# Kernel tuning notes

Measured on AMD Instinct MI355X. Metric: run time of the kernel, lower is better.

Reference implementation:

```python
import jax, jax.numpy as jnp
import numpy as np

B, S, H, M, E = 64, 512, 1024, 26, 676  # batch, seq, hidden, max_nodes, max_edges (M*M)


def setup_inputs() -> dict:
    key = jax.random.key(0)
    ks = jax.random.split(key, 16)
    seq = jax.random.normal(ks[0], (B, S, H), jnp.float32)
    # ragged, strictly-increasing sentence-end offsets in [1, S-1], zero-padded tail
    rng = np.random.RandomState(0)
    off = np.zeros((B, M - 1), np.int64)
    for b in range(B):
        c = rng.randint(5, M)  # count of valid offsets per sample (ragged)
        off[b, :c] = np.sort(rng.choice(np.arange(1, S), size=c, replace=False))
    s = 1.0 / np.sqrt(H)
    s3 = 1.0 / np.sqrt(3 * H)
    return {
        'sequence_outputs': seq,
        'proof_offsets': jnp.asarray(off),
        'node_labels': jax.random.randint(ks[1], (B, M), 0, 2),
        'edge_labels': jax.random.randint(ks[2], (B, E), 0, 2),
        'W_naf': jax.random.normal(ks[3], (H, H), jnp.float32) * s,
        'b_naf': jnp.zeros((H,), jnp.float32),
        'W_cd': jax.random.normal(ks[4], (H, H), jnp.float32) * s,
        'b_cd': jnp.zeros((H,), jnp.float32),
        'W_co': jax.random.normal(ks[5], (H, 2), jnp.float32) * s,
        'b_co': jnp.zeros((2,), jnp.float32),
        'W_nd': jax.random.normal(ks[6], (H, H), jnp.float32) * s,
        'b_nd': jnp.zeros((H,), jnp.float32),
        'W_no': jax.random.normal(ks[7], (H, 2), jnp.float32) * s,
        'b_no': jnp.zeros((2,), jnp.float32),
        'W_ed': jax.random.normal(ks[8], (3 * H, H), jnp.float32) * s3,
        'b_ed': jnp.zeros((H,), jnp.float32),
        'W_eo': jax.random.normal(ks[9], (H, 2), jnp.float32) * s,
        'b_eo': jnp.zeros((2,), jnp.float32),
    }


def reference(sequence_outputs, proof_offsets, node_labels, edge_labels,
              W_naf, b_naf, W_cd, b_cd, W_co, b_co,
              W_nd, b_nd, W_no, b_no, W_ed, b_ed, W_eo, b_eo):
    Bx, Sx, Hx = sequence_outputs.shape
    Mx = node_labels.shape[1]
    Ex = edge_labels.shape[1]

    cls = sequence_outputs[:, 0, :]                       # [B,H]
    naf = cls @ W_naf + b_naf                             # NAF node embedding
    logits = jnp.tanh(cls @ W_cd + b_cd) @ W_co + b_co    # RobertaClassificationHead (eval: dropout=id)

    # segment-mean pooling via inclusive prefix sums: segment j = tokens (prev_j, off_j]
    P = jnp.cumsum(sequence_outputs, axis=1)              # [B,S,H]
    off = proof_offsets                                   # [B,M-1]
    prev = jnp.concatenate([jnp.zeros((Bx, 1), off.dtype), off[:, :-1]], axis=1)
    valid = off > 0                                       # [B,M-1]
    seg_sum = (jnp.take_along_axis(P, off[..., None], axis=1)
               - jnp.take_along_axis(P, prev[..., None], axis=1))  # [B,M-1,H]
    seg_len = jnp.maximum(off - prev, 1).astype(sequence_outputs.dtype)
    seg_mean = seg_sum / seg_len[..., None] * valid[..., None]

    count = valid.sum(axis=1)                             # nodes per sample (excl. NAF)
    # node embeddings: seg means at 0..count-1, NAF at index count, zeros after
    node_full = jnp.concatenate([seg_mean, jnp.zeros((Bx, 1, Hx), seg_mean.dtype)], axis=1)  # [B,M,H]
    idx = jnp.arange(Mx)
    node_full = node_full + (idx[None, :, None] == count[:, None, None]) * naf[:, None, :]

    # all-pairs edge features over n=count+1 nodes, row-major flat k=i*n+j, zero-padded to E
    n = count + 1                                         # [B]
    k = jnp.arange(Ex)                                    # [E]
    i = jnp.clip(k[None, :] // n[:, None], 0, Mx - 1)     # [B,E]
    j = jnp.clip(k[None, :] % n[:, None], 0, Mx - 1)
    valid_e = (k[None, :] < (n * n)[:, None])[..., None]
    ni = jnp.take_along_axis(node_full, i[..., None], axis=1)  # [B,E,H]
    nj = jnp.take_along_axis(node_full, j[..., None], axis=1)
    edge = jnp.concatenate([nj, ni, nj - ni], axis=-1) * valid_e  # [B,E,3H]

    node_logits = jnp.tanh(node_full @ W_nd + b_nd) @ W_no + b_no
    edge_logits = jnp.tanh(edge @ W_ed + b_ed) @ W_eo + b_eo
    return (logits, node_logits, edge_logits)
```

## Files before the change

kernel.cpp:

```cpp
#include <hip/hip_runtime.h>
#include <hip/hip_bf16.h>

#define B_ 64
#define S_ 512
#define H_ 1024
#define M_ 26
#define E_ 676

typedef short bf16x8 __attribute__((ext_vector_type(8)));
typedef float f32x4 __attribute__((ext_vector_type(4)));

__device__ __forceinline__ void gload16(const void* g, void* l) {
    __builtin_amdgcn_global_load_lds((const __attribute__((address_space(1))) unsigned int*)g,
                                     (__attribute__((address_space(3))) unsigned int*)l,
                                     16, 0, 0);
}

__device__ __forceinline__ float tanh_fast(float x) {
    float e = __expf(2.0f * x);
    return 1.0f - 2.0f * __builtin_amdgcn_rcpf(e + 1.0f);
}

__global__ __launch_bounds__(256) void k_stage1(
    const float* __restrict__ seq, const int* __restrict__ off,
    const float* __restrict__ Wnaf, const float* __restrict__ Wcd,
    const float* __restrict__ Wnd, const float* __restrict__ Wed,
    const float* __restrict__ bed, const float* __restrict__ Weo,
    const float* __restrict__ beo,
    __hip_bfloat16* __restrict__ Wt, int* __restrict__ count,
    float* __restrict__ econ, float* __restrict__ naf, float* __restrict__ cdh,
    __hip_bfloat16* __restrict__ nodeB) {
    __shared__ __attribute__((aligned(16))) char smraw[20992];
    int bid = blockIdx.x;
    int tid = threadIdx.x;

    if (bid < 256) {
        __hip_bfloat16 (*ldsB)[40] = (__hip_bfloat16(*)[40])smraw;
        int* offs_s = (int*)(smraw + 20480);
        float* invL = (float*)(smraw + 20608);
        int b = bid >> 2, h0 = (bid & 3) * 256;
        int w = tid >> 6, l = tid & 63;

        if (tid < M_ - 1) offs_s[tid] = off[b * (M_ - 1) + tid];
        __syncthreads();
        int c = 0;
        while (c < M_ - 1 && offs_s[c] > 0) c++;
        int offmax = offs_s[c - 1];
        if (tid < 32)
            invL[tid] = (tid < c) ? 1.0f / (float)(offs_s[tid] - (tid ? offs_s[tid - 1] : 0))
                                  : 0.0f;
        int row0 = (l & 15), row1 = 16 + (l & 15);
        int offm0 = (row0 < c) ? offs_s[row0] : 0;
        int prv0  = (offm0 > 0) ? (row0 ? offs_s[row0 - 1] : 0) : 1;
        int offm1 = (row1 < c) ? offs_s[row1] : 0;
        int prv1  = (offm1 > 0) ? offs_s[row1 - 1] : 1;

        int nkt = (offmax >> 5) + 1;
        const float* sb = seq + (size_t)b * S_ * H_ + h0;
        float4 rg[8];
#pragma unroll
        for (int i = 0; i < 2; ++i)
#pragma unroll
            for (int r = 0; r < 4; ++r)
                rg[i * 4 + r] = *(const float4*)(sb + (size_t)((i * 4 + w) * 4 + r) * H_ + 4 * l);
        f32x4 acc[2][4] = {};
        int tA = (l >> 4) * 8;

        for (int kt = 0; kt < nkt; ++kt) {
            asm volatile("s_waitcnt vmcnt(0)" ::: "memory");
            ushort4 pk[2][4];
#pragma unroll
            for (int i = 0; i < 2; ++i)
#pragma unroll
                for (int q = 0; q < 4; ++q) {
                    float f0 = (q==0)?rg[i*4+0].x:(q==1)?rg[i*4+0].y:(q==2)?rg[i*4+0].z:rg[i*4+0].w;
                    float f1 = (q==0)?rg[i*4+1].x:(q==1)?rg[i*4+1].y:(q==2)?rg[i*4+1].z:rg[i*4+1].w;
                    float f2 = (q==0)?rg[i*4+2].x:(q==1)?rg[i*4+2].y:(q==2)?rg[i*4+2].z:rg[i*4+2].w;
                    float f3 = (q==0)?rg[i*4+3].x:(q==1)?rg[i*4+3].y:(q==2)?rg[i*4+3].z:rg[i*4+3].w;
                    __hip_bfloat16 __attribute__((aligned(8))) hh[4] = {
                        __float2bfloat16(f0), __float2bfloat16(f1),
                        __float2bfloat16(f2), __float2bfloat16(f3)};
                    pk[i][q] = *(const ushort4*)hh;
                }
            if (kt + 1 < nkt) {
#pragma unroll
                for (int i = 0; i < 2; ++i)
#pragma unroll
                    for (int r = 0; r < 4; ++r) {
                        int tl = (kt + 1) * 32 + (i * 4 + w) * 4 + r;
                        rg[i * 4 + r] = *(const float4*)(sb + (size_t)tl * H_ + 4 * l);
                    }
                __builtin_amdgcn_sched_barrier(0);
            }
#pragma unroll
            for (int i = 0; i < 2; ++i)
#pragma unroll
                for (int q = 0; q < 4; ++q)
                    *(ushort4*)&ldsB[4 * l + q][(i * 4 + w) * 4] = pk[i][q];
            asm volatile("s_waitcnt lgkmcnt(0)" ::: "memory");
            __builtin_amdgcn_s_barrier();
            int T0 = kt * 32;
            bf16x8 af0, af1;
#pragma unroll
            for (int i = 0; i < 8; ++i) {
                int t = T0 + tA + i;
                af0[i] = (t > prv0 && t <= offm0) ? (short)0x3F80 : (short)0;
                af1[i] = (t > prv1 && t <= offm1) ? (short)0x3F80 : (short)0;
            }
#pragma unroll
            for (int nn = 0; nn < 4; ++nn) {
                bf16x8 bfr = *(const bf16x8*)&ldsB[(w * 4 + nn) * 16 + (l & 15)][tA];
                acc[0][nn] = __builtin_amdgcn_mfma_f32_16x16x32_bf16(af0, bfr, acc[0][nn], 0, 0, 0);
                acc[1][nn] = __builtin_amdgcn_mfma_f32_16x16x32_bf16(af1, bfr, acc[1][nn], 0, 0, 0);
            }
            __builtin_amdgcn_s_barrier();
        }
#pragma unroll
        for (int mt = 0; mt < 2; ++mt)
#pragma unroll
            for (int nn = 0; nn < 4; ++nn) {
                f32x4 v = acc[mt][nn];
                int hcol = h0 + (w * 4 + nn) * 16 + (l & 15);
#pragma unroll
                for (int r = 0; r < 4; ++r) {
                    int m = mt * 16 + (l >> 4) * 4 + r;
                    if (m < M_)
                        nodeB[((size_t)(b * M_ + m)) * H_ + hcol] =
                            __float2bfloat16(v[r] * invL[m]);
                }
            }
    } else if (bid < 512) {
        float* smem = (float*)smraw;
        float (*As)[64] = (float(*)[64])smem;
        float (*Bs)[64] = (float(*)[64])(smem + 1024);
        int e = bid - 256;
        int bx = e & 31;
        int kbase = (e >> 5) * 128;
        const float* W;
        float* dst;
        int cbase;
        if (bx < 16) { W = Wnaf; dst = naf; cbase = bx * 64; }
        else         { W = Wcd;  dst = cdh; cbase = (bx - 16) * 64; }
        int tx = tid % 16, ty = tid / 16;
        float c[4][4] = {};
        int la_row = tid / 4;
        int la_k4  = (tid % 4) * 4;
        int lb_k   = tid / 16;
        int lb_c4  = (tid % 16) * 4;
        for (int k0 = 0; k0 < 128; k0 += 16) {
            float4 a = *(const float4*)(seq + (size_t)la_row * S_ * H_ + kbase + k0 + la_k4);
            *(float4*)(&Bs[lb_k][lb_c4]) =
                *(const float4*)(W + (size_t)(kbase + k0 + lb_k) * H_ + cbase + lb_c4);
            As[la_k4 + 0][la_row] = a.x;
            As[la_k4 + 1][la_row] = a.y;
            As[la_k4 + 2][la_row] = a.z;
            As[la_k4 + 3][la_row] = a.w;
            __syncthreads();
#pragma unroll
            for (int kk = 0; kk < 16; ++kk) {
                float4 av = *(const float4*)(&As[kk][ty * 4]);
                float4 bv = *(const float4*)(&Bs[kk][tx * 4]);
                c[0][0] += av.x * bv.x; c[0][1] += av.x * bv.y; c[0][2] += av.x * bv.z; c[0][3] += av.x * bv.w;
                c[1][0] += av.y * bv.x; c[1][1] += av.y * bv.y; c[1][2] += av.y * bv.z; c[1][3] += av.y * bv.w;
                c[2][0] += av.z * bv.x; c[2][1] += av.z * bv.y; c[2][2] += av.z * bv.z; c[2][3] += av.z * bv.w;
                c[3][0] += av.w * bv.x; c[3][1] += av.w * bv.y; c[3][2] += av.w * bv.z; c[3][3] += av.w * bv.w;
            }
            __syncthreads();
        }
#pragma unroll
        for (int i = 0; i < 4; ++i)
#pragma unroll
            for (int j = 0; j < 4; ++j)
                atomicAdd(dst + (size_t)(ty * 4 + i) * H_ + cbase + tx * 4 + j, c[i][j]);
    } else if (bid < 3584) {
        float (*T)[33] = (float(*)[33])smraw;
        int idx = bid - 512;
        int s = idx >> 10, rem = idx & 1023;
        int bx = rem & 31, by = rem >> 5;
        int c = tid & 31, r0 = tid >> 5;
        const int HH = H_ * H_;
#pragma unroll
        for (int i = 0; i < 4; ++i) {
            int r = r0 + 8 * i;
            size_t k = by * 32 + r, n = bx * 32 + c;
            float v;
            if (s == 0)      v = Wnd[k * H_ + n];
            else if (s == 1) v = Wed[k * H_ + n] + Wed[2 * HH + k * H_ + n];
            else             v = Wed[HH + k * H_ + n] - Wed[2 * HH + k * H_ + n];
            T[r][c] = v;
        }
        __syncthreads();
#pragma unroll
        for (int i = 0; i < 4; ++i) {
            int rr = r0 + 8 * i;
            Wt[(size_t)(s * H_ + bx * 32 + rr) * H_ + by * 32 + c] = __float2bfloat16(T[c][rr]);
        }
    } else if (bid == 3584) {
        if (tid < 64) {
            int b = tid;
            int c = 0;
            for (int m = 0; m < M_ - 1; ++m) c += (off[b * (M_ - 1) + m] > 0) ? 1 : 0;
            count[b] = c;
        }
    } else {
        float* s0 = (float*)smraw; float* s1 = (float*)smraw + 256;
        float a0 = 0.f, a1 = 0.f;
        for (int h = tid; h < H_; h += 256) {
            float t = tanh_fast(bed[h]);
            a0 += t * Weo[h * 2 + 0];
            a1 += t * Weo[h * 2 + 1];
        }
        s0[tid] = a0; s1[tid] = a1; __syncthreads();
        for (int o = 128; o > 0; o >>= 1) {
            if (tid < o) { s0[tid] += s0[tid + o]; s1[tid] += s1[tid + o]; }
            __syncthreads();
        }
        if (tid == 0) { econ[0] = s0[0] + beo[0]; econ[1] = s1[0] + beo[1]; }
    }
}

__global__ __launch_bounds__(256) void k_stage2s(
    const float* __restrict__ naf, const float* __restrict__ bnaf,
    const int* __restrict__ count, __hip_bfloat16* __restrict__ nodeB,
    const float* __restrict__ cdh, const float* __restrict__ bcd,
    const float* __restrict__ Wco, const float* __restrict__ bco,
    float* __restrict__ out) {
    __shared__ float smem[512];
    int bid = blockIdx.x;
    int tid = threadIdx.x;
    if (bid < 64) {
        int b = bid, cnt = count[b];
        float4 a = ((const float4*)(naf + (size_t)b * H_))[tid];
        float4 bb = ((const float4*)bnaf)[tid];
        __hip_bfloat16 __attribute__((aligned(8))) h[4] = {
            __float2bfloat16(a.x + bb.x), __float2bfloat16(a.y + bb.y),
            __float2bfloat16(a.z + bb.z), __float2bfloat16(a.w + bb.w)};
        *(ushort4*)(nodeB + ((size_t)(b * M_ + cnt)) * H_ + tid * 4) = *(const ushort4*)h;
    } else {
        int b = bid - 64;
        float* s0 = smem; float* s1 = smem + 256;
        float a0 = 0.f, a1 = 0.f;
        for (int h = tid; h < H_; h += 256) {
            float t = tanh_fast(cdh[(size_t)b * H_ + h] + bcd[h]);
            a0 += t * Wco[h * 2 + 0];
            a1 += t * Wco[h * 2 + 1];
        }
        s0[tid] = a0; s1[tid] = a1; __syncthreads();
        for (int o = 128; o > 0; o >>= 1) {
            if (tid < o) { s0[tid] += s0[tid + o]; s1[tid] += s1[tid + o]; }
            __syncthreads();
        }
        if (tid == 0) { out[b * 2 + 0] = s0[0] + bco[0]; out[b * 2 + 1] = s1[0] + bco[1]; }
    }
}

#define GM 1664
#define GN 3072
#define GK 1024
__global__ __launch_bounds__(256) void k_mfma(const __hip_bfloat16* __restrict__ A,
                                              const __hip_bfloat16* __restrict__ Bt,
                                              float* __restrict__ C) {
    __shared__ __hip_bfloat16 As[128 * 32];
    __shared__ __hip_bfloat16 Bs[128 * 32];
    int tid = threadIdx.x;
    int wid = tid >> 6, ln = tid & 63;
    int row0 = blockIdx.y * 128, col0 = blockIdx.x * 128;
    const __hip_bfloat16* ga = A + (size_t)(row0 + wid * 16 + (ln >> 2)) * GK + (ln & 3) * 8;
    const __hip_bfloat16* gb = Bt + (size_t)(col0 + wid * 16 + (ln >> 2)) * GK + (ln & 3) * 8;
    __hip_bfloat16* lA = As + wid * 512;
    __hip_bfloat16* lB = Bs + wid * 512;
    int mrow = (wid >> 1) * 64, ncol = (wid & 1) * 64;
    int l15 = ln & 15, l4 = ln >> 4;
    f32x4 acc[4][4] = {};
    const __hip_bfloat16* pa = As + (size_t)(mrow + l15) * 32 + l4 * 8;
    const __hip_bfloat16* pb = Bs + (size_t)(ncol + l15) * 32 + l4 * 8;
    for (int k0 = 0; k0 < GK; k0 += 32) {
        gload16(ga, lA);
        gload16(ga + 64 * GK, lA + 2048);
        gload16(gb, lB);
        gload16(gb + 64 * GK, lB + 2048);
        ga += 32; gb += 32;
        __syncthreads();
        bf16x8 af[4], bf[4];
#pragma unroll
        for (int mi = 0; mi < 4; ++mi) af[mi] = *(const bf16x8*)(pa + mi * 16 * 32);
#pragma unroll
        for (int ni = 0; ni < 4; ++ni) bf[ni] = *(const bf16x8*)(pb + ni * 16 * 32);
#pragma unroll
        for (int mi = 0; mi < 4; ++mi)
#pragma unroll
            for (int ni = 0; ni < 4; ++ni)
                acc[mi][ni] = __builtin_amdgcn_mfma_f32_16x16x32_bf16(af[mi], bf[ni],
                                                                      acc[mi][ni], 0, 0, 0);
        __syncthreads();
    }
#pragma unroll
    for (int mi = 0; mi < 4; ++mi)
#pragma unroll
        for (int ni = 0; ni < 4; ++ni) {
            f32x4 v = acc[mi][ni];
            size_t r = row0 + mrow + mi * 16 + l4 * 4;
            size_t cc = col0 + ncol + ni * 16 + l15;
            C[(r + 0) * GN + cc] = v[0];
            C[(r + 1) * GN + cc] = v[1];
            C[(r + 2) * GN + cc] = v[2];
            C[(r + 3) * GN + cc] = v[3];
        }
}

__global__ __launch_bounds__(256) void k_stage4(
    const float* __restrict__ Cm, const int* __restrict__ count,
    const float* __restrict__ bnd, const float* __restrict__ Wno,
    const float* __restrict__ bno, const float* __restrict__ bed,
    const float* __restrict__ Weo, const float* __restrict__ beo,
    const float* __restrict__ econ, float* __restrict__ out_n,
    float* __restrict__ out_e) {
    int bid = blockIdx.x;
    int wid = threadIdx.x >> 6, lane = threadIdx.x & 63;
    if (bid < 416) {
        int r = bid * 4 + wid;
        const float4* src = (const float4*)(Cm + (size_t)r * GN);
        float a0 = 0.f, a1 = 0.f;
#pragma unroll
        for (int it = 0; it < 4; ++it) {
            int h = lane * 4 + it * 256;
            float4 s = src[lane + it * 64];
            float4 bb = *(const float4*)(bnd + h);
            float t0 = tanh_fast(s.x + bb.x), t1 = tanh_fast(s.y + bb.y);
            float t2 = tanh_fast(s.z + bb.z), t3 = tanh_fast(s.w + bb.w);
            a0 += t0 * Wno[h * 2 + 0] + t1 * Wno[h * 2 + 2] + t2 * Wno[h * 2 + 4] + t3 * Wno[h * 2 + 6];
            a1 += t0 * Wno[h * 2 + 1] + t1 * Wno[h * 2 + 3] + t2 * Wno[h * 2 + 5] + t3 * Wno[h * 2 + 7];
        }
        for (int o = 32; o > 0; o >>= 1) { a0 += __shfl_down(a0, o); a1 += __shfl_down(a1, o); }
        if (lane == 0) { out_n[(size_t)r * 2 + 0] = a0 + bno[0]; out_n[(size_t)r * 2 + 1] = a1 + bno[1]; }
    } else {
        int e = bid - 416;
        int b = e >> 4;
        int wg = (e & 15) * 4 + wid;
        int n = count[b] + 1;
        int n2 = n * n;
        float4 bed4[4], w04[4], w14[4];
#pragma unroll
        for (int it = 0; it < 4; ++it) {
            int h = lane * 4 + it * 256;
            bed4[it] = *(const float4*)(bed + h);
            w04[it] = make_float4(Weo[h * 2 + 0], Weo[h * 2 + 2], Weo[h * 2 + 4], Weo[h * 2 + 6]);
            w14[it] = make_float4(Weo[h * 2 + 1], Weo[h * 2 + 3], Weo[h * 2 + 5], Weo[h * 2 + 7]);
        }
        float e0 = econ[0], e1 = econ[1];
        float b0 = beo[0], b1 = beo[1];
        for (int k = wg; k < E_; k += 64) {
            float* dst = out_e + ((size_t)b * E_ + k) * 2;
            if (k >= n2) {
                if (lane == 0) { dst[0] = e0; dst[1] = e1; }
                continue;
            }
            int i = k / n, j = k - i * n;
            const float4* U4 = (const float4*)(Cm + (size_t)(b * M_ + j) * GN + H_);
            const float4* V4 = (const float4*)(Cm + (size_t)(b * M_ + i) * GN + 2 * H_);
            float a0 = 0.f, a1 = 0.f;
#pragma unroll
            for (int it = 0; it < 4; ++it) {
                float4 u = U4[lane + it * 64];
                float4 v = V4[lane + it * 64];
                float t0 = tanh_fast(u.x + v.x + bed4[it].x);
                float t1 = tanh_fast(u.y + v.y + bed4[it].y);
                float t2 = tanh_fast(u.z + v.z + bed4[it].z);
                float t3 = tanh_fast(u.w + v.w + bed4[it].w);
                a0 += t0 * w04[it].x + t1 * w04[it].y + t2 * w04[it].z + t3 * w04[it].w;
                a1 += t0 * w14[it].x + t1 * w14[it].y + t2 * w14[it].z + t3 * w14[it].w;
            }
            for (int o = 32; o > 0; o >>= 1) { a0 += __shfl_down(a0, o); a1 += __shfl_down(a1, o); }
            if (lane == 0) { dst[0] = a0 + b0; dst[1] = a1 + b1; }
        }
    }
}

extern "C" void kernel_launch(void* const* d_in, const int* in_sizes, int n_in,
                              void* d_out, int out_size, void* d_ws, size_t ws_size,
                              hipStream_t stream) {
    const float* seq  = (const float*)d_in[0];
    const int*   off  = (const int*)d_in[1];
    const float* Wnaf = (const float*)d_in[4];  const float* bnaf = (const float*)d_in[5];
    const float* Wcd  = (const float*)d_in[6];  const float* bcd  = (const float*)d_in[7];
    const float* Wco  = (const float*)d_in[8];  const float* bco  = (const float*)d_in[9];
    const float* Wnd  = (const float*)d_in[10]; const float* bnd  = (const float*)d_in[11];
    const float* Wno  = (const float*)d_in[12]; const float* bno  = (const float*)d_in[13];
    const float* Wed  = (const float*)d_in[14]; const float* bed  = (const float*)d_in[15];
    const float* Weo  = (const float*)d_in[16]; const float* beo  = (const float*)d_in[17];
    float* out = (float*)d_out;

    float* ws = (float*)d_ws;
    size_t p = 0;
    float* naf   = ws + p;  p += (size_t)B_ * H_;
    float* cdh   = ws + p;  p += (size_t)B_ * H_;
    __hip_bfloat16* nodeB = (__hip_bfloat16*)(ws + p); p += (size_t)B_ * M_ * H_ / 2;
    __hip_bfloat16* Wt    = (__hip_bfloat16*)(ws + p); p += (size_t)3 * H_ * H_ / 2;
    float* Cbuf  = ws + p;  p += (size_t)GM * GN;
    int*   cnt   = (int*)(ws + p); p += 64;
    float* econ  = ws + p;  p += 2;

    hipMemsetAsync(naf, 0, 2 * (size_t)B_ * H_ * sizeof(float), stream);

    k_stage1<<<dim3(3586), 256, 0, stream>>>(seq, off, Wnaf, Wcd, Wnd, Wed, bed, Weo, beo,
                                             Wt, cnt, econ, naf, cdh, nodeB);
    k_stage2s<<<dim3(128), 256, 0, stream>>>(naf, bnaf, cnt, nodeB,
                                             cdh, bcd, Wco, bco, out);
    k_mfma<<<dim3(GN / 128, GM / 128), 256, 0, stream>>>(nodeB, Wt, Cbuf);
    k_stage4<<<dim3(1440), 256, 0, stream>>>(Cbuf, cnt, bnd, Wno, bno, bed, Weo, beo, econ,
                                             out + B_ * 2, out + B_ * 2 + B_ * M_ * 2);
}
```

Measured before the change: 310.4 us.

## Compact valid node rows in GEMM via rowmap and replace atomics with split-K partials

Builds a per-sample prefix base and a rowmap so the bf16 MFMA GEMM only processes the count+1 valid node rows per sample. Blocks whose row tile lies past the total return early, and padded node rows get a precomputed constant logit (tanh(b_nd)·W_no+b_no). The naf/cdh split-K reduction now writes 8 partial buffers with plain float4 stores instead of atomics, which also removes the memset. Costs are an indirect row gather in the GEMM A loads and extra partial-sum reads in stage 2.

```diff
diff --git a/kernel.cpp b/kernel.cpp
--- a/kernel.cpp
+++ b/kernel.cpp
@@ -26,9 +26,12 @@
     const float* __restrict__ Wnaf, const float* __restrict__ Wcd,
     const float* __restrict__ Wnd, const float* __restrict__ Wed,
     const float* __restrict__ bed, const float* __restrict__ Weo,
-    const float* __restrict__ beo,
+    const float* __restrict__ beo, const float* __restrict__ bnd,
+    const float* __restrict__ Wno, const float* __restrict__ bno,
     __hip_bfloat16* __restrict__ Wt, int* __restrict__ count,
-    float* __restrict__ econ, float* __restrict__ naf, float* __restrict__ cdh,
+    int* __restrict__ base, int* __restrict__ rowmap,
+    float* __restrict__ econ, float* __restrict__ nconst,
+    float* __restrict__ naf8, float* __restrict__ cdh8,
     __hip_bfloat16* __restrict__ nodeB) {
     __shared__ __attribute__((aligned(16))) char smraw[20992];
     int bid = blockIdx.x;
@@ -124,7 +127,7 @@
 #pragma unroll
                 for (int r = 0; r < 4; ++r) {
                     int m = mt * 16 + (l >> 4) * 4 + r;
-                    if (m < M_)
+                    if (m < c)
                         nodeB[((size_t)(b * M_ + m)) * H_ + hcol] =
                             __float2bfloat16(v[r] * invL[m]);
                 }
@@ -135,12 +138,13 @@
         float (*Bs)[64] = (float(*)[64])(smem + 1024);
         int e = bid - 256;
         int bx = e & 31;
-        int kbase = (e >> 5) * 128;
+        int kg = e >> 5;
+        int kbase = kg * 128;
         const float* W;
         float* dst;
         int cbase;
-        if (bx < 16) { W = Wnaf; dst = naf; cbase = bx * 64; }
-        else         { W = Wcd;  dst = cdh; cbase = (bx - 16) * 64; }
+        if (bx < 16) { W = Wnaf; dst = naf8 + (size_t)kg * 64 * H_; cbase = bx * 64; }
+        else         { W = Wcd;  dst = cdh8 + (size_t)kg * 64 * H_; cbase = (bx - 16) * 64; }
         int tx = tid % 16, ty = tid / 16;
         float c[4][4] = {};
         int la_row = tid / 4;
@@ -168,10 +172,10 @@
             __syncthreads();
         }
 #pragma unroll
-        for (int i = 0; i < 4; ++i)
-#pragma unroll
-            for (int j = 0; j < 4; ++j)
-                atomicAdd(dst + (size_t)(ty * 4 + i) * H_ + cbase + tx * 4 + j, c[i][j]);
+        for (int i = 0; i < 4; ++i) {
+            float4 v = make_float4(c[i][0], c[i][1], c[i][2], c[i][3]);
+            *(float4*)(dst + (size_t)(ty * 4 + i) * H_ + cbase + tx * 4) = v;
+        }
     } else if (bid < 3584) {
         float (*T)[33] = (float(*)[33])smraw;
         int idx = bid - 512;
@@ -196,11 +200,24 @@
             Wt[(size_t)(s * H_ + bx * 32 + rr) * H_ + by * 32 + c] = __float2bfloat16(T[c][rr]);
         }
     } else if (bid == 3584) {
+        int* cnt_s = (int*)smraw;
+        int* base_s = (int*)smraw + 64;
         if (tid < 64) {
-            int b = tid;
-            int c = 0;
+            int b = tid, c = 0;
             for (int m = 0; m < M_ - 1; ++m) c += (off[b * (M_ - 1) + m] > 0) ? 1 : 0;
-            count[b] = c;
+            cnt_s[b] = c; count[b] = c;
+        }
+        __syncthreads();
+        if (tid == 0) {
+            int a = 0;
+            for (int b = 0; b < 64; ++b) { base_s[b] = a; a += cnt_s[b] + 1; }
+            base_s[64] = a;
+        }
+        __syncthreads();
+        if (tid < 65) base[tid] = base_s[tid];
+        if (tid < 64) {
+            int b = tid, bs = base_s[b];
+            for (int m = 0; m <= cnt_s[b]; ++m) rowmap[bs + m] = b * M_ + m;
         }
     } else {
         float* s0 = (float*)smraw; float* s1 = (float*)smraw + 256;
@@ -216,21 +233,39 @@
             __syncthreads();
         }
         if (tid == 0) { econ[0] = s0[0] + beo[0]; econ[1] = s1[0] + beo[1]; }
+        __syncthreads();
+        a0 = 0.f; a1 = 0.f;
+        for (int h = tid; h < H_; h += 256) {
+            float t = tanh_fast(bnd[h]);
+            a0 += t * Wno[h * 2 + 0];
+            a1 += t * Wno[h * 2 + 1];
+        }
+        s0[tid] = a0; s1[tid] = a1; __syncthreads();
+        for (int o = 128; o > 0; o >>= 1) {
+            if (tid < o) { s0[tid] += s0[tid + o]; s1[tid] += s1[tid + o]; }
+            __syncthreads();
+        }
+        if (tid == 0) { nconst[0] = s0[0] + bno[0]; nconst[1] = s1[0] + bno[1]; }
     }
 }
 
 __global__ __launch_bounds__(256) void k_stage2s(
-    const float* __restrict__ naf, const float* __restrict__ bnaf,
-    const int* __restrict__ count, __hip_bfloat16* __restrict__ nodeB,
-    const float* __restrict__ cdh, const float* __restrict__ bcd,
-    const float* __restrict__ Wco, const float* __restrict__ bco,
-    float* __restrict__ out) {
+    const float* __restrict__ naf8, const float* __restrict__ cdh8,
+    const float* __restrict__ bnaf, const int* __restrict__ count,
+    __hip_bfloat16* __restrict__ nodeB,
+    const float* __restrict__ bcd, const float* __restrict__ Wco,
+    const float* __restrict__ bco, float* __restrict__ out) {
     __shared__ float smem[512];
     int bid = blockIdx.x;
     int tid = threadIdx.x;
     if (bid < 64) {
         int b = bid, cnt = count[b];
-        float4 a = ((const float4*)(naf + (size_t)b * H_))[tid];
+        float4 a = make_float4(0.f, 0.f, 0.f, 0.f);
+#pragma unroll
+        for (int kg = 0; kg < 8; ++kg) {
+            float4 s = ((const float4*)(naf8 + (size_t)kg * 64 * H_ + (size_t)b * H_))[tid];
+            a.x += s.x; a.y += s.y; a.z += s.z; a.w += s.w;
+        }
         float4 bb = ((const float4*)bnaf)[tid];
         __hip_bfloat16 __attribute__((aligned(8))) h[4] = {
             __float2bfloat16(a.x + bb.x), __float2bfloat16(a.y + bb.y),
@@ -241,7 +276,10 @@
         float* s0 = smem; float* s1 = smem + 256;
         float a0 = 0.f, a1 = 0.f;
         for (int h = tid; h < H_; h += 256) {
-            float t = tanh_fast(cdh[(size_t)b * H_ + h] + bcd[h]);
+            float v = 0.f;
+#pragma unroll
+            for (int kg = 0; kg < 8; ++kg) v += cdh8[(size_t)kg * 64 * H_ + (size_t)b * H_ + h];
+            float t = tanh_fast(v + bcd[h]);
             a0 += t * Wco[h * 2 + 0];
             a1 += t * Wco[h * 2 + 1];
         }
@@ -259,13 +297,21 @@
 #define GK 1024
 __global__ __launch_bounds__(256) void k_mfma(const __hip_bfloat16* __restrict__ A,
                                               const __hip_bfloat16* __restrict__ Bt,
-                                              float* __restrict__ C) {
+                                              float* __restrict__ C,
+                                              const int* __restrict__ rowmap,
+                                              const int* __restrict__ base) {
     __shared__ __hip_bfloat16 As[128 * 32];
     __shared__ __hip_bfloat16 Bs[128 * 32];
+    int rowtotal = base[64];
+    int row0 = blockIdx.y * 128;
+    if (row0 >= rowtotal) return;
     int tid = threadIdx.x;
     int wid = tid >> 6, ln = tid & 63;
-    int row0 = blockIdx.y * 128, col0 = blockIdx.x * 128;
-    const __hip_bfloat16* ga = A + (size_t)(row0 + wid * 16 + (ln >> 2)) * GK + (ln & 3) * 8;
+    int col0 = blockIdx.x * 128;
+    int ai0 = row0 + wid * 16 + (ln >> 2);      if (ai0 > rowtotal - 1) ai0 = rowtotal - 1;
+    int ai1 = row0 + 64 + wid * 16 + (ln >> 2); if (ai1 > rowtotal - 1) ai1 = rowtotal - 1;
+    const __hip_bfloat16* ga0 = A + (size_t)rowmap[ai0] * GK + (ln & 3) * 8;
+    const __hip_bfloat16* ga1 = A + (size_t)rowmap[ai1] * GK + (ln & 3) * 8;
     const __hip_bfloat16* gb = Bt + (size_t)(col0 + wid * 16 + (ln >> 2)) * GK + (ln & 3) * 8;
     __hip_bfloat16* lA = As + wid * 512;
     __hip_bfloat16* lB = Bs + wid * 512;
@@ -275,11 +321,11 @@
     const __hip_bfloat16* pa = As + (size_t)(mrow + l15) * 32 + l4 * 8;
     const __hip_bfloat16* pb = Bs + (size_t)(ncol + l15) * 32 + l4 * 8;
     for (int k0 = 0; k0 < GK; k0 += 32) {
-        gload16(ga, lA);
-        gload16(ga + 64 * GK, lA + 2048);
+        gload16(ga0, lA);
+        gload16(ga1, lA + 2048);
         gload16(gb, lB);
         gload16(gb + 64 * GK, lB + 2048);
-        ga += 32; gb += 32;
+        ga0 += 32; ga1 += 32; gb += 32;
         __syncthreads();
         bf16x8 af[4], bf[4];
 #pragma unroll
@@ -299,46 +345,53 @@
 #pragma unroll
         for (int ni = 0; ni < 4; ++ni) {
             f32x4 v = acc[mi][ni];
-            size_t r = row0 + mrow + mi * 16 + l4 * 4;
+            int r = row0 + mrow + mi * 16 + l4 * 4;
             size_t cc = col0 + ncol + ni * 16 + l15;
-            C[(r + 0) * GN + cc] = v[0];
-            C[(r + 1) * GN + cc] = v[1];
-            C[(r + 2) * GN + cc] = v[2];
-            C[(r + 3) * GN + cc] = v[3];
+#pragma unroll
+            for (int j = 0; j < 4; ++j)
+                if (r + j < rowtotal) C[(size_t)(r + j) * GN + cc] = v[j];
         }
 }
 
 __global__ __launch_bounds__(256) void k_stage4(
     const float* __restrict__ Cm, const int* __restrict__ count,
-    const float* __restrict__ bnd, const float* __restrict__ Wno,
-    const float* __restrict__ bno, const float* __restrict__ bed,
-    const float* __restrict__ Weo, const float* __restrict__ beo,
-    const float* __restrict__ econ, float* __restrict__ out_n,
+    const int* __restrict__ base, const float* __restrict__ bnd,
+    const float* __restrict__ Wno, const float* __restrict__ bno,
+    const float* __restrict__ bed, const float* __restrict__ Weo,
+    const float* __restrict__ beo, const float* __restrict__ econ,
+    const float* __restrict__ nconst, float* __restrict__ out_n,
     float* __restrict__ out_e) {
     int bid = blockIdx.x;
     int wid = threadIdx.x >> 6, lane = threadIdx.x & 63;
     if (bid < 416) {
         int r = bid * 4 + wid;
-        const float4* src = (const float4*)(Cm + (size_t)r * GN);
-        float a0 = 0.f, a1 = 0.f;
-#pragma unroll
-        for (int it = 0; it < 4; ++it) {
-            int h = lane * 4 + it * 256;
-            float4 s = src[lane + it * 64];
-            float4 bb = *(const float4*)(bnd + h);
-            float t0 = tanh_fast(s.x + bb.x), t1 = tanh_fast(s.y + bb.y);
-            float t2 = tanh_fast(s.z + bb.z), t3 = tanh_fast(s.w + bb.w);
-            a0 += t0 * Wno[h * 2 + 0] + t1 * Wno[h * 2 + 2] + t2 * Wno[h * 2 + 4] + t3 * Wno[h * 2 + 6];
-            a1 += t0 * Wno[h * 2 + 1] + t1 * Wno[h * 2 + 3] + t2 * Wno[h * 2 + 5] + t3 * Wno[h * 2 + 7];
-        }
-        for (int o = 32; o > 0; o >>= 1) { a0 += __shfl_down(a0, o); a1 += __shfl_down(a1, o); }
-        if (lane == 0) { out_n[(size_t)r * 2 + 0] = a0 + bno[0]; out_n[(size_t)r * 2 + 1] = a1 + bno[1]; }
+        int b = r / 26, m = r - b * 26;
+        if (m <= count[b]) {
+            const float4* src = (const float4*)(Cm + (size_t)(base[b] + m) * GN);
+            float a0 = 0.f, a1 = 0.f;
+#pragma unroll
+            for (int it = 0; it < 4; ++it) {
+                int h = lane * 4 + it * 256;
+                float4 s = src[lane + it * 64];
+                float4 bb = *(const float4*)(bnd + h);
+                float t0 = tanh_fast(s.x + bb.x), t1 = tanh_fast(s.y + bb.y);
+                float t2 = tanh_fast(s.z + bb.z), t3 = tanh_fast(s.w + bb.w);
+                a0 += t0 * Wno[h * 2 + 0] + t1 * Wno[h * 2 + 2] + t2 * Wno[h * 2 + 4] + t3 * Wno[h * 2 + 6];
+                a1 += t0 * Wno[h * 2 + 1] + t1 * Wno[h * 2 + 3] + t2 * Wno[h * 2 + 5] + t3 * Wno[h * 2 + 7];
+            }
+            for (int o = 32; o > 0; o >>= 1) { a0 += __shfl_down(a0, o); a1 += __shfl_down(a1, o); }
+            if (lane == 0) { out_n[(size_t)r * 2 + 0] = a0 + bno[0]; out_n[(size_t)r * 2 + 1] = a1 + bno[1]; }
+        } else if (lane == 0) {
+            out_n[(size_t)r * 2 + 0] = nconst[0];
+            out_n[(size_t)r * 2 + 1] = nconst[1];
+        }
     } else {
         int e = bid - 416;
         int b = e >> 4;
         int wg = (e & 15) * 4 + wid;
         int n = count[b] + 1;
         int n2 = n * n;
+        int bb_ = base[b];
         float4 bed4[4], w04[4], w14[4];
 #pragma unroll
         for (int it = 0; it < 4; ++it) {
@@ -356,8 +409,8 @@
                 continue;
             }
             int i = k / n, j = k - i * n;
-            const float4* U4 = (const float4*)(Cm + (size_t)(b * M_ + j) * GN + H_);
-            const float4* V4 = (const float4*)(Cm + (size_t)(b * M_ + i) * GN + 2 * H_);
+            const float4* U4 = (const float4*)(Cm + (size_t)(bb_ + j) * GN + H_);
+            const float4* V4 = (const float4*)(Cm + (size_t)(bb_ + i) * GN + 2 * H_);
             float a0 = 0.f, a1 = 0.f;
 #pragma unroll
             for (int it = 0; it < 4; ++it) {
@@ -392,21 +445,25 @@
 
     float* ws = (float*)d_ws;
     size_t p = 0;
-    float* naf   = ws + p;  p += (size_t)B_ * H_;
-    float* cdh   = ws + p;  p += (size_t)B_ * H_;
+    float* naf8  = ws + p;  p += (size_t)8 * 64 * H_;
+    float* cdh8  = ws + p;  p += (size_t)8 * 64 * H_;
     __hip_bfloat16* nodeB = (__hip_bfloat16*)(ws + p); p += (size_t)B_ * M_ * H_ / 2;
     __hip_bfloat16* Wt    = (__hip_bfloat16*)(ws + p); p += (size_t)3 * H_ * H_ / 2;
     float* Cbuf  = ws + p;  p += (size_t)GM * GN;
     int*   cnt   = (int*)(ws + p); p += 64;
+    int*   base  = (int*)(ws + p); p += 65;
+    int*   rowmap = (int*)(ws + p); p += GM;
     float* econ  = ws + p;  p += 2;
-
-    hipMemsetAsync(naf, 0, 2 * (size_t)B_ * H_ * sizeof(float), stream);
+    float* nconst = ws + p; p += 2;
+
 
     k_stage1<<<dim3(3586), 256, 0, stream>>>(seq, off, Wnaf, Wcd, Wnd, Wed, bed, Weo, beo,
-                                             Wt, cnt, econ, naf, cdh, nodeB);
-    k_stage2s<<<dim3(128), 256, 0, stream>>>(naf, bnaf, cnt, nodeB,
-                                             cdh, bcd, Wco, bco, out);
-    k_mfma<<<dim3(GN / 128, GM / 128), 256, 0, stream>>>(nodeB, Wt, Cbuf);
-    k_stage4<<<dim3(1440), 256, 0, stream>>>(Cbuf, cnt, bnd, Wno, bno, bed, Weo, beo, econ,
+                                             bnd, Wno, bno, Wt, cnt, base, rowmap,
+                                             econ, nconst, naf8, cdh8, nodeB);
+    k_stage2s<<<dim3(128), 256, 0, stream>>>(naf8, cdh8, bnaf, cnt, nodeB,
+                                             bcd, Wco, bco, out);
+    k_mfma<<<dim3(GN / 128, GM / 128), 256, 0, stream>>>(nodeB, Wt, Cbuf, rowmap, base);
+    k_stage4<<<dim3(1440), 256, 0, stream>>>(Cbuf, cnt, base, bnd, Wno, bno, bed, Weo, beo,
+                                             econ, nconst,
                                              out + B_ * 2, out + B_ * 2 + B_ * M_ * 2);
 }
```

After: 301.5 us. -2.8%, faster.
